# Kernel tuning notes

Hardware: AMD Instinct MI355X
Metric: run time of the kernel (lower is better)

Reference implementation:

```python
import jax, jax.numpy as jnp
import numpy as np

D_MODEL = 512
N_HEADS = 8
D_HEAD = 64
D_FF = 1024
EPS = 1e-5


def setup_inputs() -> dict:
    key = jax.random.key(0)
    ks = jax.random.split(key, 9)
    B, L = 4, 2048
    s = lambda fan_in: 1.0 / np.sqrt(fan_in)
    return {
        "x": jax.random.normal(ks[0], (B, L, D_MODEL), dtype=jnp.float32),
        "ln1_w": jnp.ones((D_MODEL,), jnp.float32),
        "ln1_b": jnp.zeros((D_MODEL,), jnp.float32),
        "ln2_w": jnp.ones((D_MODEL,), jnp.float32),
        "ln2_b": jnp.zeros((D_MODEL,), jnp.float32),
        "wq": jax.random.normal(ks[1], (D_MODEL, N_HEADS * D_HEAD), jnp.float32) * s(D_MODEL),
        "wk": jax.random.normal(ks[2], (D_MODEL, N_HEADS * D_HEAD), jnp.float32) * s(D_MODEL),
        "wv": jax.random.normal(ks[3], (D_MODEL, N_HEADS * D_HEAD), jnp.float32) * s(D_MODEL),
        "wo": jax.random.normal(ks[4], (N_HEADS * D_HEAD, D_MODEL), jnp.float32) * s(N_HEADS * D_HEAD),
        "w_gate": jax.random.normal(ks[5], (D_MODEL, D_FF), jnp.float32) * s(D_MODEL),
        "w_up": jax.random.normal(ks[6], (D_MODEL, D_FF), jnp.float32) * s(D_MODEL),
        "w_down": jax.random.normal(ks[7], (D_FF, D_MODEL), jnp.float32) * s(D_FF),
    }


def _layernorm(x, w, b):
    mu = jnp.mean(x, axis=-1, keepdims=True)
    var = jnp.var(x, axis=-1, keepdims=True)
    return (x - mu) * jax.lax.rsqrt(var + EPS) * w + b


def reference(x, ln1_w, ln1_b, ln2_w, ln2_b, wq, wk, wv, wo, w_gate, w_up, w_down):
    B, L, _ = x.shape
    scale = D_HEAD ** -0.5

    # --- attention sublayer (pre-LN residual) ---
    h = _layernorm(x, ln1_w, ln1_b)
    q = (h @ wq).reshape(B, L, N_HEADS, D_HEAD)  # [B,L,H,Dh]
    k = (h @ wk).reshape(B, L, N_HEADS, D_HEAD)
    v = (h @ wv).reshape(B, L, N_HEADS, D_HEAD)
    scores = jnp.einsum("bqhd,bkhd->bhqk", q, k) * scale
    # softmax computed in fp32, cast back (matches F.softmax(dtype=float32).to(q.dtype))
    attn = jax.nn.softmax(scores.astype(jnp.float32), axis=-1).astype(q.dtype)
    out = jnp.einsum("bhqk,bkhd->bqhd", attn, v).reshape(B, L, N_HEADS * D_HEAD)
    x = x + out @ wo

    # --- SwiGLU FFN sublayer (pre-LN residual) ---
    h = _layernorm(x, ln2_w, ln2_b)
    gate = jax.nn.silu(h @ w_gate)
    x = x + (gate * (h @ w_up)) @ w_down
    return x
```

## Files before the change

### kernel.cpp

```cpp
#include <hip/hip_runtime.h>
#include <hip/hip_bf16.h>
#include <math.h>

#define EPS 1e-5f

typedef __attribute__((ext_vector_type(8))) short bf16x8;
typedef __attribute__((ext_vector_type(4))) float f32x4;

__device__ __forceinline__ short f2bf(float x) {
    union { float f; unsigned u; } un; un.f = x;
    unsigned r = un.u + 0x7FFF + ((un.u >> 16) & 1);
    return (short)(r >> 16);
}
__device__ __forceinline__ float bf2f(short s) {
    union { unsigned u; float f; } un;
    un.u = ((unsigned)(unsigned short)s) << 16;
    return un.f;
}
__device__ __forceinline__ unsigned pack_bf2(float a, float b) {
    unsigned r;
    asm("v_cvt_pk_bf16_f32 %0, %1, %2" : "=v"(r) : "v"(a), "v"(b));
    return r;
}
__device__ __forceinline__ float exp2_fast(float x) {
    float r;
    asm("v_exp_f32 %0, %1" : "=v"(r) : "v"(x));
    return r;
}
__device__ __forceinline__ void load_lds16(const short* g, short* l) {
    __builtin_amdgcn_global_load_lds(
        (const __attribute__((address_space(1))) unsigned int*)g,
        (__attribute__((address_space(3))) unsigned int*)l, 16, 0, 0);
}

__global__ __launch_bounds__(256) void ln_kernel_b(const float* __restrict__ in,
                                                   const float* __restrict__ w,
                                                   const float* __restrict__ bb,
                                                   short* __restrict__ out) {
    int wv = threadIdx.x >> 6, lane = threadIdx.x & 63;
    int row = blockIdx.x * 4 + wv;
    const float* x = in + (size_t)row * 512 + lane * 8;
    float4 v0 = *(const float4*)x;
    float4 v1 = *(const float4*)(x + 4);
    float s  = (v0.x + v0.y) + (v0.z + v0.w) + (v1.x + v1.y) + (v1.z + v1.w);
    float s2 = v0.x*v0.x + v0.y*v0.y + v0.z*v0.z + v0.w*v0.w
             + v1.x*v1.x + v1.y*v1.y + v1.z*v1.z + v1.w*v1.w;
#pragma unroll
    for (int off = 1; off < 64; off <<= 1) {
        s  += __shfl_xor(s, off);
        s2 += __shfl_xor(s2, off);
    }
    float mu = s * (1.f / 512.f);
    float rstd = rsqrtf(s2 * (1.f / 512.f) - mu * mu + EPS);
    const float4 wa = *(const float4*)&w[lane * 8];
    const float4 wb = *(const float4*)&w[lane * 8 + 4];
    const float4 ba = *(const float4*)&bb[lane * 8];
    const float4 bv = *(const float4*)&bb[lane * 8 + 4];
    uint4 o;
    o.x = pack_bf2((v0.x - mu) * rstd * wa.x + ba.x, (v0.y - mu) * rstd * wa.y + ba.y);
    o.y = pack_bf2((v0.z - mu) * rstd * wa.z + ba.z, (v0.w - mu) * rstd * wa.w + ba.w);
    o.z = pack_bf2((v1.x - mu) * rstd * wb.x + bv.x, (v1.y - mu) * rstd * wb.y + bv.y);
    o.w = pack_bf2((v1.z - mu) * rstd * wb.z + bv.z, (v1.w - mu) * rstd * wb.w + bv.w);
    *(uint4*)&out[(size_t)row * 512 + lane * 8] = o;
}

struct WT { const float* w; short* t; int K; int N; };
struct WT7 { WT a[7]; };
__global__ __launch_bounds__(256) void transp_w_kernel(WT7 p) {
    WT e = p.a[blockIdx.z];
    int k0 = blockIdx.x * 32, n0 = blockIdx.y * 32;
    if (k0 >= e.K || n0 >= e.N) return;
    __shared__ short t[32][33];
    int tx = threadIdx.x & 31, ty = threadIdx.x >> 5;
#pragma unroll
    for (int pp = 0; pp < 4; pp++)
        t[pp * 8 + ty][tx] = f2bf(e.w[(size_t)(k0 + pp * 8 + ty) * e.N + n0 + tx]);
    __syncthreads();
#pragma unroll
    for (int pp = 0; pp < 4; pp++)
        e.t[(size_t)(n0 + pp * 8 + ty) * e.K + k0 + tx] = t[tx][pp * 8 + ty];
}

template <int EPI>
__global__ __launch_bounds__(256) void gemm_mfma(const short* __restrict__ A,
                                                 const short* __restrict__ Bt,
                                                 const float* __restrict__ res,
                                                 const short* __restrict__ resb,
                                                 void* __restrict__ Cv,
                                                 int M, int N, int K) {
    __shared__ short As[128 * 64];
    __shared__ short Bs[128 * 64];
    const int tid = threadIdx.x;
    const int lane = tid & 63, w = tid >> 6;
    const int g = lane >> 4, r16 = lane & 15;
    const int wr = w >> 1, wc = w & 1;

    const int nb = gridDim.x * gridDim.y;
    const int fid = blockIdx.y * gridDim.x + blockIdx.x;
    const int nid = (fid & 7) * (nb >> 3) + (fid >> 3);
    const int m0 = (nid / gridDim.x) * 128, n0 = (nid % gridDim.x) * 128;

    const int lr = lane >> 3;
    const int ck = (lane & 7) ^ lr;
    const int row0 = w * 32;

    f32x4 acc[4][4] = {};

    for (int k0 = 0; k0 < K; k0 += 64) {
        __syncthreads();
#pragma unroll
        for (int p = 0; p < 4; p++) {
            int rb = row0 + p * 8;
            load_lds16(&A [(size_t)(m0 + rb + lr) * K + k0 + ck * 8], &As[rb * 64]);
            load_lds16(&Bt[(size_t)(n0 + rb + lr) * K + k0 + ck * 8], &Bs[rb * 64]);
        }
        __syncthreads();
#pragma unroll
        for (int ks = 0; ks < 2; ks++) {
            bf16x8 av[4], bv[4];
#pragma unroll
            for (int i = 0; i < 4; i++) {
                int row = wr * 64 + i * 16 + r16;
                av[i] = *(const bf16x8*)&As[row * 64 + ((ks * 4 + g) ^ (row & 7)) * 8];
            }
#pragma unroll
            for (int j = 0; j < 4; j++) {
                int row = wc * 64 + j * 16 + r16;
                bv[j] = *(const bf16x8*)&Bs[row * 64 + ((ks * 4 + g) ^ (row & 7)) * 8];
            }
#pragma unroll
            for (int i = 0; i < 4; i++)
#pragma unroll
                for (int j = 0; j < 4; j++)
                    acc[i][j] = __builtin_amdgcn_mfma_f32_16x16x32_bf16(av[i], bv[j], acc[i][j], 0, 0, 0);
        }
    }

#pragma unroll
    for (int i = 0; i < 4; i++)
#pragma unroll
        for (int j = 0; j < 4; j++)
#pragma unroll
            for (int jr = 0; jr < 4; jr++) {
                int m = m0 + wr * 64 + i * 16 + 4 * g + jr;
                int n = n0 + wc * 64 + j * 16 + r16;
                float v = acc[i][j][jr];
                if (EPI == 0) {
                    size_t idx = (size_t)m * N + n;
                    ((float*)Cv)[idx] = res[idx] + v;
                } else if (EPI == 1) {
                    ((short*)Cv)[(size_t)m * N + n] = f2bf(v);
                } else if (EPI == 2) {
                    if (n < 512) v *= 0.18033688011112042f;
                    ((short*)Cv)[(size_t)(n >> 9) * 4194304 +
                                 (((size_t)(m >> 11) * 8 + ((n >> 6) & 7)) * 2048 + (m & 2047)) * 64 + (n & 63)] = f2bf(v);
                } else {
                    float gt = bf2f(resb[(size_t)m * N + n]);
                    float y = gt / (1.f + __expf(-gt)) * v;
                    ((short*)Cv)[(size_t)m * N + n] = f2bf(y);
                }
            }
}

__global__ __launch_bounds__(256) void transp_v_kernel(const short* __restrict__ vb,
                                                       short* __restrict__ vt) {
    __shared__ short tile[64][65];
    int l0 = blockIdx.x * 64;
    int bh = blockIdx.y;
    const size_t base = (size_t)bh * 2048 * 64;
    int tid = threadIdx.x;
#pragma unroll
    for (int p = 0; p < 4; p++) {
        int r = p * 16 + (tid >> 4);
        int c4 = (tid & 15) * 4;
        *(short4*)&tile[r][c4] = *(const short4*)&vb[base + (size_t)(l0 + r) * 64 + c4];
    }
    __syncthreads();
#pragma unroll
    for (int p = 0; p < 4; p++) {
        int d = p * 16 + (tid >> 4);
        int c4 = (tid & 15) * 4;
        short4 o;
        o.x = tile[c4 + 0][d]; o.y = tile[c4 + 1][d];
        o.z = tile[c4 + 2][d]; o.w = tile[c4 + 3][d];
        *(short4*)&vt[base + (size_t)d * 2048 + l0 + c4] = o;
    }
}

__global__ __launch_bounds__(256) void attn_mfma_kernel(const short* __restrict__ qb,
                                                        const short* __restrict__ kb,
                                                        const short* __restrict__ vt,
                                                        short* __restrict__ outb) {
    __shared__ short QP[128 * 64];
    __shared__ short Ks[2][4096];
    __shared__ short Vs[2][4096];

    const int fid = blockIdx.y * gridDim.x + blockIdx.x;
    const int nid = (fid & 7) * 64 + (fid >> 3);
    const int bh = nid >> 4, qt = nid & 15;
    const int b = bh >> 3, h = bh & 7;
    const int q0 = qt * 128;
    const size_t hb = (size_t)bh * (2048 * 64);

    const int tid = threadIdx.x;
    const int lane = tid & 63, w = tid >> 6;
    const int g = lane >> 4, r16 = lane & 15;
    const int lr = lane >> 3, ck = (lane & 7) ^ lr;
    const int rx = r16 & 7;

#pragma unroll
    for (int p = 0; p < 4; p++)
        load_lds16(&qb[hb + (size_t)(q0 + 32 * w + 8 * p + lr) * 64 + ck * 8],
                   &QP[(32 * w + 8 * p) * 64]);

    auto stageKV = [&](int buf, int kt) {
        int k0 = kt * 64;
        int rb = w * 16;
        load_lds16(&kb[hb + (size_t)(k0 + rb + lr) * 64 + ck * 8],      &Ks[buf][rb * 64]);
        load_lds16(&kb[hb + (size_t)(k0 + rb + 8 + lr) * 64 + ck * 8],  &Ks[buf][(rb + 8) * 64]);
        load_lds16(&vt[hb + (size_t)(rb + lr) * 2048 + k0 + ck * 8],     &Vs[buf][rb * 64]);
        load_lds16(&vt[hb + (size_t)(rb + 8 + lr) * 2048 + k0 + ck * 8], &Vs[buf][(rb + 8) * 64]);
    };
    stageKV(0, 0);

    bf16x8 aqA0, aqA1, aqB0, aqB1;
    float mA = -1e30f, lA = 0.f, mB = -1e30f, lB = 0.f;
    f32x4 oA[4] = {}, oB[4] = {};
    int cur = 0;

    for (int t = 0; t < 32; t++) {
        __syncthreads();
        if (t == 0) {
            int rowA = 32 * w + r16, rowB = rowA + 16;
            aqA0 = *(const bf16x8*)&QP[rowA * 64 + ((0 + g) ^ rx) * 8];
            aqA1 = *(const bf16x8*)&QP[rowA * 64 + ((4 + g) ^ rx) * 8];
            aqB0 = *(const bf16x8*)&QP[rowB * 64 + ((0 + g) ^ rx) * 8];
            aqB1 = *(const bf16x8*)&QP[rowB * 64 + ((4 + g) ^ rx) * 8];
        }
        if (t + 1 < 32) stageKV(cur ^ 1, t + 1);
        const short* Kc = &Ks[cur][0];
        const short* Vc = &Vs[cur][0];

        f32x4 sA[4], sB[4];
#pragma unroll
        for (int c = 0; c < 4; c++) {
            int row = 16 * c + r16;
            bf16x8 ak0 = *(const bf16x8*)&Kc[row * 64 + ((0 + g) ^ rx) * 8];
            bf16x8 ak1 = *(const bf16x8*)&Kc[row * 64 + ((4 + g) ^ rx) * 8];
            f32x4 a1 = {}, a2 = {};
            a1 = __builtin_amdgcn_mfma_f32_16x16x32_bf16(ak0, aqA0, a1, 0, 0, 0);
            a1 = __builtin_amdgcn_mfma_f32_16x16x32_bf16(ak1, aqA1, a1, 0, 0, 0);
            a2 = __builtin_amdgcn_mfma_f32_16x16x32_bf16(ak0, aqB0, a2, 0, 0, 0);
            a2 = __builtin_amdgcn_mfma_f32_16x16x32_bf16(ak1, aqB1, a2, 0, 0, 0);
            sA[c] = a1; sB[c] = a2;
        }

        float pmA = sA[0][0], pmB = sB[0][0];
#pragma unroll
        for (int c = 0; c < 4; c++)
#pragma unroll
            for (int jr = 0; jr < 4; jr++) {
                if (c || jr) {
                    pmA = fmaxf(pmA, sA[c][jr]);
                    pmB = fmaxf(pmB, sB[c][jr]);
                }
            }
        pmA = fmaxf(pmA, __shfl_xor(pmA, 16));
        pmA = fmaxf(pmA, __shfl_xor(pmA, 32));
        pmB = fmaxf(pmB, __shfl_xor(pmB, 16));
        pmB = fmaxf(pmB, __shfl_xor(pmB, 32));
        if (!__all((pmA - mA <= 8.f) && (pmB - mB <= 8.f))) {
            float mnA = fmaxf(mA, pmA), mnB = fmaxf(mB, pmB);
            float alA = exp2_fast(mA - mnA), alB = exp2_fast(mB - mnB);
            lA *= alA; lB *= alB;
#pragma unroll
            for (int c = 0; c < 4; c++) { oA[c] *= alA; oB[c] *= alB; }
            mA = mnA; mB = mnB;
        }
        float rsA = 0.f, rsB = 0.f;
        int prA = 32 * w + r16, prB = prA + 16;
#pragma unroll
        for (int c = 0; c < 4; c++) {
            int colbase = 16 * c + 4 * g;
            int co = (((colbase >> 3) ^ rx) * 8) + (colbase & 7);
            {
                float p0 = exp2_fast(sA[c][0] - mA), p1 = exp2_fast(sA[c][1] - mA);
                float p2 = exp2_fast(sA[c][2] - mA), p3 = exp2_fast(sA[c][3] - mA);
                rsA += (p0 + p1) + (p2 + p3);
                unsigned long long pv = (unsigned long long)pack_bf2(p0, p1)
                                      | ((unsigned long long)pack_bf2(p2, p3) << 32);
                *(unsigned long long*)&QP[prA * 64 + co] = pv;
            }
            {
                float p0 = exp2_fast(sB[c][0] - mB), p1 = exp2_fast(sB[c][1] - mB);
                float p2 = exp2_fast(sB[c][2] - mB), p3 = exp2_fast(sB[c][3] - mB);
                rsB += (p0 + p1) + (p2 + p3);
                unsigned long long pv = (unsigned long long)pack_bf2(p0, p1)
                                      | ((unsigned long long)pack_bf2(p2, p3) << 32);
                *(unsigned long long*)&QP[prB * 64 + co] = pv;
            }
        }
        rsA += __shfl_xor(rsA, 16); rsA += __shfl_xor(rsA, 32); lA += rsA;
        rsB += __shfl_xor(rsB, 16); rsB += __shfl_xor(rsB, 32); lB += rsB;

        bf16x8 bpA0 = *(const bf16x8*)&QP[prA * 64 + ((0 + g) ^ rx) * 8];
        bf16x8 bpA1 = *(const bf16x8*)&QP[prA * 64 + ((4 + g) ^ rx) * 8];
        bf16x8 bpB0 = *(const bf16x8*)&QP[prB * 64 + ((0 + g) ^ rx) * 8];
        bf16x8 bpB1 = *(const bf16x8*)&QP[prB * 64 + ((4 + g) ^ rx) * 8];
#pragma unroll
        for (int c = 0; c < 4; c++) {
            int row = 16 * c + r16;
            bf16x8 av0 = *(const bf16x8*)&Vc[row * 64 + ((0 + g) ^ rx) * 8];
            bf16x8 av1 = *(const bf16x8*)&Vc[row * 64 + ((4 + g) ^ rx) * 8];
            oA[c] = __builtin_amdgcn_mfma_f32_16x16x32_bf16(av0, bpA0, oA[c], 0, 0, 0);
            oA[c] = __builtin_amdgcn_mfma_f32_16x16x32_bf16(av1, bpA1, oA[c], 0, 0, 0);
            oB[c] = __builtin_amdgcn_mfma_f32_16x16x32_bf16(av0, bpB0, oB[c], 0, 0, 0);
            oB[c] = __builtin_amdgcn_mfma_f32_16x16x32_bf16(av1, bpB1, oB[c], 0, 0, 0);
        }
        cur ^= 1;
    }

    float ivA = 1.f / lA, ivB = 1.f / lB;
    int qa = q0 + 32 * w + r16;
#pragma unroll
    for (int c = 0; c < 4; c++) {
        int d = 16 * c + 4 * g;
        {
            unsigned long long pv = (unsigned long long)pack_bf2(oA[c][0] * ivA, oA[c][1] * ivA)
                                  | ((unsigned long long)pack_bf2(oA[c][2] * ivA, oA[c][3] * ivA) << 32);
            *(unsigned long long*)&outb[((size_t)b * 2048 + qa) * 512 + h * 64 + d] = pv;
        }
        {
            unsigned long long pv = (unsigned long long)pack_bf2(oB[c][0] * ivB, oB[c][1] * ivB)
                                  | ((unsigned long long)pack_bf2(oB[c][2] * ivB, oB[c][3] * ivB) << 32);
            *(unsigned long long*)&outb[((size_t)b * 2048 + qa + 16) * 512 + h * 64 + d] = pv;
        }
    }
}

extern "C" void kernel_launch(void* const* d_in, const int* in_sizes, int n_in,
                              void* d_out, int out_size, void* d_ws, size_t ws_size,
                              hipStream_t stream) {
    const float* x      = (const float*)d_in[0];
    const float* ln1_w  = (const float*)d_in[1];
    const float* ln1_b  = (const float*)d_in[2];
    const float* ln2_w  = (const float*)d_in[3];
    const float* ln2_b  = (const float*)d_in[4];
    const float* wq     = (const float*)d_in[5];
    const float* wk     = (const float*)d_in[6];
    const float* wv     = (const float*)d_in[7];
    const float* wo     = (const float*)d_in[8];
    const float* w_gate = (const float*)d_in[9];
    const float* w_up   = (const float*)d_in[10];
    const float* w_down = (const float*)d_in[11];
    float* out = (float*)d_out;

    const int M = 4 * 2048;
    char* ws = (char*)d_ws;
    const size_t MB = 1 << 20;
    short* h1b   = (short*)(ws);
    short* qb    = (short*)(ws + 8 * MB);
    short* kb    = (short*)(ws + 16 * MB);
    short* vb    = (short*)(ws + 24 * MB);
    short* vt    = (short*)(ws + 32 * MB);
    short* aob   = (short*)(ws + 40 * MB);
    short* g_b   = (short*)(ws + 48 * MB);
    short* u_b   = (short*)(ws + 64 * MB);
    short* qkvT  = (short*)(ws + 80 * MB);
    short* woT   = (short*)(ws + 82 * MB);
    short* wguT  = (short*)(ws + 83 * MB);
    short* wdT   = (short*)(ws + 85 * MB);
    short* h2b   = qb;

    WT7 wt;
    wt.a[0] = {wq,     qkvT,               512,  512};
    wt.a[1] = {wk,     qkvT + 512 * 512,   512,  512};
    wt.a[2] = {wv,     qkvT + 1024 * 512,  512,  512};
    wt.a[3] = {wo,     woT,                512,  512};
    wt.a[4] = {w_gate, wguT,               512, 1024};
    wt.a[5] = {w_up,   wguT + 1024 * 512,  512, 1024};
    wt.a[6] = {w_down, wdT,               1024,  512};

    transp_w_kernel<<<dim3(32, 32, 7), 256, 0, stream>>>(wt);
    ln_kernel_b<<<M / 4, 256, 0, stream>>>(x, ln1_w, ln1_b, h1b);
    gemm_mfma<2><<<dim3(12, 64), 256, 0, stream>>>(h1b, qkvT, nullptr, nullptr, qb, M, 1536, 512);
    transp_v_kernel<<<dim3(32, 32), 256, 0, stream>>>(vb, vt);
    attn_mfma_kernel<<<dim3(16, 32), 256, 0, stream>>>(qb, kb, vt, aob);
    gemm_mfma<0><<<dim3(4, 64), 256, 0, stream>>>(aob, woT, x, nullptr, out, M, 512, 512);
    ln_kernel_b<<<M / 4, 256, 0, stream>>>(out, ln2_w, ln2_b, h2b);
    gemm_mfma<1><<<dim3(8, 64), 256, 0, stream>>>(h2b, wguT, nullptr, nullptr, g_b, M, 1024, 512);
    gemm_mfma<4><<<dim3(8, 64), 256, 0, stream>>>(h2b, wguT + 1024 * 512, nullptr, g_b, u_b, M, 1024, 512);
    gemm_mfma<0><<<dim3(4, 64), 256, 0, stream>>>(u_b, wdT, out, nullptr, out, M, 512, 1024);
}
```

Before: 183.1 us.

## Double-buffer GEMM LDS tiles and software-pipeline attention PV MFMAs

The GEMM kernel now double-buffers its A/B LDS tiles and prefetches the next K tile while computing the current one, with one waitcnt+barrier per iteration instead of two syncthreads. The attention kernel defers the P·V MFMAs to the next iteration, holding V fragments and P in registers so they overlap with the next QK^T and softmax. It also drops the lazy-rescale threshold and always rescales. The cost is higher register and LDS pressure, which may lower occupancy, plus an unconditional rescale every tile.

```diff
diff --git a/kernel.cpp b/kernel.cpp
--- a/kernel.cpp
+++ b/kernel.cpp
@@ -6,6 +6,8 @@
 
 typedef __attribute__((ext_vector_type(8))) short bf16x8;
 typedef __attribute__((ext_vector_type(4))) float f32x4;
+
+#define MFMA16 __builtin_amdgcn_mfma_f32_16x16x32_bf16
 
 __device__ __forceinline__ short f2bf(float x) {
     union { float f; unsigned u; } un; un.f = x;
@@ -31,6 +33,11 @@
     __builtin_amdgcn_global_load_lds(
         (const __attribute__((address_space(1))) unsigned int*)g,
         (__attribute__((address_space(3))) unsigned int*)l, 16, 0, 0);
+}
+__device__ __forceinline__ void wait_vm0_barrier() {
+    asm volatile("s_waitcnt vmcnt(0)" ::: "memory");
+    __builtin_amdgcn_s_barrier();
+    __builtin_amdgcn_sched_barrier(0);
 }
 
 __global__ __launch_bounds__(256) void ln_kernel_b(const float* __restrict__ in,
@@ -88,8 +95,8 @@
                                                  const short* __restrict__ resb,
                                                  void* __restrict__ Cv,
                                                  int M, int N, int K) {
-    __shared__ short As[128 * 64];
-    __shared__ short Bs[128 * 64];
+    __shared__ short As[2][128 * 64];
+    __shared__ short Bs[2][128 * 64];
     const int tid = threadIdx.x;
     const int lane = tid & 63, w = tid >> 6;
     const int g = lane >> 4, r16 = lane & 15;
@@ -104,36 +111,44 @@
     const int ck = (lane & 7) ^ lr;
     const int row0 = w * 32;
 
-    f32x4 acc[4][4] = {};
-
-    for (int k0 = 0; k0 < K; k0 += 64) {
-        __syncthreads();
+    auto stage = [&](int buf, int k0) {
 #pragma unroll
         for (int p = 0; p < 4; p++) {
             int rb = row0 + p * 8;
-            load_lds16(&A [(size_t)(m0 + rb + lr) * K + k0 + ck * 8], &As[rb * 64]);
-            load_lds16(&Bt[(size_t)(n0 + rb + lr) * K + k0 + ck * 8], &Bs[rb * 64]);
-        }
-        __syncthreads();
+            load_lds16(&A [(size_t)(m0 + rb + lr) * K + k0 + ck * 8], &As[buf][rb * 64]);
+            load_lds16(&Bt[(size_t)(n0 + rb + lr) * K + k0 + ck * 8], &Bs[buf][rb * 64]);
+        }
+    };
+
+    f32x4 acc[4][4] = {};
+    stage(0, 0);
+    wait_vm0_barrier();
+
+    const int nt = K >> 6;
+    int cur = 0;
+    for (int t = 0; t < nt; t++) {
+        if (t + 1 < nt) stage(cur ^ 1, (t + 1) << 6);
 #pragma unroll
         for (int ks = 0; ks < 2; ks++) {
             bf16x8 av[4], bv[4];
 #pragma unroll
             for (int i = 0; i < 4; i++) {
                 int row = wr * 64 + i * 16 + r16;
-                av[i] = *(const bf16x8*)&As[row * 64 + ((ks * 4 + g) ^ (row & 7)) * 8];
+                av[i] = *(const bf16x8*)&As[cur][row * 64 + ((ks * 4 + g) ^ (row & 7)) * 8];
             }
 #pragma unroll
             for (int j = 0; j < 4; j++) {
                 int row = wc * 64 + j * 16 + r16;
-                bv[j] = *(const bf16x8*)&Bs[row * 64 + ((ks * 4 + g) ^ (row & 7)) * 8];
+                bv[j] = *(const bf16x8*)&Bs[cur][row * 64 + ((ks * 4 + g) ^ (row & 7)) * 8];
             }
 #pragma unroll
             for (int i = 0; i < 4; i++)
 #pragma unroll
                 for (int j = 0; j < 4; j++)
-                    acc[i][j] = __builtin_amdgcn_mfma_f32_16x16x32_bf16(av[i], bv[j], acc[i][j], 0, 0, 0);
-        }
+                    acc[i][j] = MFMA16(av[i], bv[j], acc[i][j], 0, 0, 0);
+        }
+        wait_vm0_barrier();
+        cur ^= 1;
     }
 
 #pragma unroll
@@ -222,21 +237,22 @@
         load_lds16(&vt[hb + (size_t)(rb + 8 + lr) * 2048 + k0 + ck * 8], &Vs[buf][(rb + 8) * 64]);
     };
     stageKV(0, 0);
-
-    bf16x8 aqA0, aqA1, aqB0, aqB1;
+    wait_vm0_barrier();
+
+    const int rowA = 32 * w + r16, rowB = rowA + 16;
+    bf16x8 aqA0 = *(const bf16x8*)&QP[rowA * 64 + ((0 + g) ^ rx) * 8];
+    bf16x8 aqA1 = *(const bf16x8*)&QP[rowA * 64 + ((4 + g) ^ rx) * 8];
+    bf16x8 aqB0 = *(const bf16x8*)&QP[rowB * 64 + ((0 + g) ^ rx) * 8];
+    bf16x8 aqB1 = *(const bf16x8*)&QP[rowB * 64 + ((4 + g) ^ rx) * 8];
+
     float mA = -1e30f, lA = 0.f, mB = -1e30f, lB = 0.f;
+    float alA = 1.f, alB = 1.f;
     f32x4 oA[4] = {}, oB[4] = {};
+    bf16x8 vf0, vf1, vf2, vf3, vf4, vf5, vf6, vf7;
+    bf16x8 pfA0, pfA1, pfB0, pfB1;
     int cur = 0;
 
     for (int t = 0; t < 32; t++) {
-        __syncthreads();
-        if (t == 0) {
-            int rowA = 32 * w + r16, rowB = rowA + 16;
-            aqA0 = *(const bf16x8*)&QP[rowA * 64 + ((0 + g) ^ rx) * 8];
-            aqA1 = *(const bf16x8*)&QP[rowA * 64 + ((4 + g) ^ rx) * 8];
-            aqB0 = *(const bf16x8*)&QP[rowB * 64 + ((0 + g) ^ rx) * 8];
-            aqB1 = *(const bf16x8*)&QP[rowB * 64 + ((4 + g) ^ rx) * 8];
-        }
         if (t + 1 < 32) stageKV(cur ^ 1, t + 1);
         const short* Kc = &Ks[cur][0];
         const short* Vc = &Vs[cur][0];
@@ -248,37 +264,49 @@
             bf16x8 ak0 = *(const bf16x8*)&Kc[row * 64 + ((0 + g) ^ rx) * 8];
             bf16x8 ak1 = *(const bf16x8*)&Kc[row * 64 + ((4 + g) ^ rx) * 8];
             f32x4 a1 = {}, a2 = {};
-            a1 = __builtin_amdgcn_mfma_f32_16x16x32_bf16(ak0, aqA0, a1, 0, 0, 0);
-            a1 = __builtin_amdgcn_mfma_f32_16x16x32_bf16(ak1, aqA1, a1, 0, 0, 0);
-            a2 = __builtin_amdgcn_mfma_f32_16x16x32_bf16(ak0, aqB0, a2, 0, 0, 0);
-            a2 = __builtin_amdgcn_mfma_f32_16x16x32_bf16(ak1, aqB1, a2, 0, 0, 0);
+            a1 = MFMA16(ak0, aqA0, a1, 0, 0, 0);
+            a1 = MFMA16(ak1, aqA1, a1, 0, 0, 0);
+            a2 = MFMA16(ak0, aqB0, a2, 0, 0, 0);
+            a2 = MFMA16(ak1, aqB1, a2, 0, 0, 0);
             sA[c] = a1; sB[c] = a2;
         }
 
-        float pmA = sA[0][0], pmB = sB[0][0];
-#pragma unroll
-        for (int c = 0; c < 4; c++)
-#pragma unroll
-            for (int jr = 0; jr < 4; jr++) {
-                if (c || jr) {
-                    pmA = fmaxf(pmA, sA[c][jr]);
-                    pmB = fmaxf(pmB, sB[c][jr]);
-                }
-            }
-        pmA = fmaxf(pmA, __shfl_xor(pmA, 16));
-        pmA = fmaxf(pmA, __shfl_xor(pmA, 32));
-        pmB = fmaxf(pmB, __shfl_xor(pmB, 16));
-        pmB = fmaxf(pmB, __shfl_xor(pmB, 32));
-        if (!__all((pmA - mA <= 8.f) && (pmB - mB <= 8.f))) {
-            float mnA = fmaxf(mA, pmA), mnB = fmaxf(mB, pmB);
-            float alA = exp2_fast(mA - mnA), alB = exp2_fast(mB - mnB);
-            lA *= alA; lB *= alB;
+        if (t > 0) {
 #pragma unroll
             for (int c = 0; c < 4; c++) { oA[c] *= alA; oB[c] *= alB; }
-            mA = mnA; mB = mnB;
-        }
+            oA[0] = MFMA16(vf0, pfA0, oA[0], 0, 0, 0); oA[0] = MFMA16(vf1, pfA1, oA[0], 0, 0, 0);
+            oB[0] = MFMA16(vf0, pfB0, oB[0], 0, 0, 0); oB[0] = MFMA16(vf1, pfB1, oB[0], 0, 0, 0);
+            oA[1] = MFMA16(vf2, pfA0, oA[1], 0, 0, 0); oA[1] = MFMA16(vf3, pfA1, oA[1], 0, 0, 0);
+            oB[1] = MFMA16(vf2, pfB0, oB[1], 0, 0, 0); oB[1] = MFMA16(vf3, pfB1, oB[1], 0, 0, 0);
+            oA[2] = MFMA16(vf4, pfA0, oA[2], 0, 0, 0); oA[2] = MFMA16(vf5, pfA1, oA[2], 0, 0, 0);
+            oB[2] = MFMA16(vf4, pfB0, oB[2], 0, 0, 0); oB[2] = MFMA16(vf5, pfB1, oB[2], 0, 0, 0);
+            oA[3] = MFMA16(vf6, pfA0, oA[3], 0, 0, 0); oA[3] = MFMA16(vf7, pfA1, oA[3], 0, 0, 0);
+            oB[3] = MFMA16(vf6, pfB0, oB[3], 0, 0, 0); oB[3] = MFMA16(vf7, pfB1, oB[3], 0, 0, 0);
+        }
+
+        vf0 = *(const bf16x8*)&Vc[(r16     ) * 64 + ((0 + g) ^ rx) * 8];
+        vf1 = *(const bf16x8*)&Vc[(r16     ) * 64 + ((4 + g) ^ rx) * 8];
+        vf2 = *(const bf16x8*)&Vc[(16 + r16) * 64 + ((0 + g) ^ rx) * 8];
+        vf3 = *(const bf16x8*)&Vc[(16 + r16) * 64 + ((4 + g) ^ rx) * 8];
+        vf4 = *(const bf16x8*)&Vc[(32 + r16) * 64 + ((0 + g) ^ rx) * 8];
+        vf5 = *(const bf16x8*)&Vc[(32 + r16) * 64 + ((4 + g) ^ rx) * 8];
+        vf6 = *(const bf16x8*)&Vc[(48 + r16) * 64 + ((0 + g) ^ rx) * 8];
+        vf7 = *(const bf16x8*)&Vc[(48 + r16) * 64 + ((4 + g) ^ rx) * 8];
+
+        float pmA = fmaxf(fmaxf(sA[0][0], sA[0][1]), fmaxf(sA[0][2], sA[0][3]));
+        float pmB = fmaxf(fmaxf(sB[0][0], sB[0][1]), fmaxf(sB[0][2], sB[0][3]));
+#pragma unroll
+        for (int c = 1; c < 4; c++) {
+            pmA = fmaxf(pmA, fmaxf(fmaxf(sA[c][0], sA[c][1]), fmaxf(sA[c][2], sA[c][3])));
+            pmB = fmaxf(pmB, fmaxf(fmaxf(sB[c][0], sB[c][1]), fmaxf(sB[c][2], sB[c][3])));
+        }
+        pmA = fmaxf(pmA, __shfl_xor(pmA, 16)); pmA = fmaxf(pmA, __shfl_xor(pmA, 32));
+        pmB = fmaxf(pmB, __shfl_xor(pmB, 16)); pmB = fmaxf(pmB, __shfl_xor(pmB, 32));
+        float mnA = fmaxf(mA, pmA), mnB = fmaxf(mB, pmB);
+        alA = exp2_fast(mA - mnA); alB = exp2_fast(mB - mnB);
+        mA = mnA; mB = mnB;
+        lA *= alA; lB *= alB;
         float rsA = 0.f, rsB = 0.f;
-        int prA = 32 * w + r16, prB = prA + 16;
 #pragma unroll
         for (int c = 0; c < 4; c++) {
             int colbase = 16 * c + 4 * g;
@@ -289,7 +317,7 @@
                 rsA += (p0 + p1) + (p2 + p3);
                 unsigned long long pv = (unsigned long long)pack_bf2(p0, p1)
                                       | ((unsigned long long)pack_bf2(p2, p3) << 32);
-                *(unsigned long long*)&QP[prA * 64 + co] = pv;
+                *(unsigned long long*)&QP[rowA * 64 + co] = pv;
             }
             {
                 float p0 = exp2_fast(sB[c][0] - mB), p1 = exp2_fast(sB[c][1] - mB);
@@ -297,28 +325,31 @@
                 rsB += (p0 + p1) + (p2 + p3);
                 unsigned long long pv = (unsigned long long)pack_bf2(p0, p1)
                                       | ((unsigned long long)pack_bf2(p2, p3) << 32);
-                *(unsigned long long*)&QP[prB * 64 + co] = pv;
+                *(unsigned long long*)&QP[rowB * 64 + co] = pv;
             }
         }
         rsA += __shfl_xor(rsA, 16); rsA += __shfl_xor(rsA, 32); lA += rsA;
         rsB += __shfl_xor(rsB, 16); rsB += __shfl_xor(rsB, 32); lB += rsB;
 
-        bf16x8 bpA0 = *(const bf16x8*)&QP[prA * 64 + ((0 + g) ^ rx) * 8];
-        bf16x8 bpA1 = *(const bf16x8*)&QP[prA * 64 + ((4 + g) ^ rx) * 8];
-        bf16x8 bpB0 = *(const bf16x8*)&QP[prB * 64 + ((0 + g) ^ rx) * 8];
-        bf16x8 bpB1 = *(const bf16x8*)&QP[prB * 64 + ((4 + g) ^ rx) * 8];
-#pragma unroll
-        for (int c = 0; c < 4; c++) {
-            int row = 16 * c + r16;
-            bf16x8 av0 = *(const bf16x8*)&Vc[row * 64 + ((0 + g) ^ rx) * 8];
-            bf16x8 av1 = *(const bf16x8*)&Vc[row * 64 + ((4 + g) ^ rx) * 8];
-            oA[c] = __builtin_amdgcn_mfma_f32_16x16x32_bf16(av0, bpA0, oA[c], 0, 0, 0);
-            oA[c] = __builtin_amdgcn_mfma_f32_16x16x32_bf16(av1, bpA1, oA[c], 0, 0, 0);
-            oB[c] = __builtin_amdgcn_mfma_f32_16x16x32_bf16(av0, bpB0, oB[c], 0, 0, 0);
-            oB[c] = __builtin_amdgcn_mfma_f32_16x16x32_bf16(av1, bpB1, oB[c], 0, 0, 0);
-        }
+        pfA0 = *(const bf16x8*)&QP[rowA * 64 + ((0 + g) ^ rx) * 8];
+        pfA1 = *(const bf16x8*)&QP[rowA * 64 + ((4 + g) ^ rx) * 8];
+        pfB0 = *(const bf16x8*)&QP[rowB * 64 + ((0 + g) ^ rx) * 8];
+        pfB1 = *(const bf16x8*)&QP[rowB * 64 + ((4 + g) ^ rx) * 8];
+
+        wait_vm0_barrier();
         cur ^= 1;
     }
+
+#pragma unroll
+    for (int c = 0; c < 4; c++) { oA[c] *= alA; oB[c] *= alB; }
+    oA[0] = MFMA16(vf0, pfA0, oA[0], 0, 0, 0); oA[0] = MFMA16(vf1, pfA1, oA[0], 0, 0, 0);
+    oB[0] = MFMA16(vf0, pfB0, oB[0], 0, 0, 0); oB[0] = MFMA16(vf1, pfB1, oB[0], 0, 0, 0);
+    oA[1] = MFMA16(vf2, pfA0, oA[1], 0, 0, 0); oA[1] = MFMA16(vf3, pfA1, oA[1], 0, 0, 0);
+    oB[1] = MFMA16(vf2, pfB0, oB[1], 0, 0, 0); oB[1] = MFMA16(vf3, pfB1, oB[1], 0, 0, 0);
+    oA[2] = MFMA16(vf4, pfA0, oA[2], 0, 0, 0); oA[2] = MFMA16(vf5, pfA1, oA[2], 0, 0, 0);
+    oB[2] = MFMA16(vf4, pfB0, oB[2], 0, 0, 0); oB[2] = MFMA16(vf5, pfB1, oB[2], 0, 0, 0);
+    oA[3] = MFMA16(vf6, pfA0, oA[3], 0, 0, 0); oA[3] = MFMA16(vf7, pfA1, oA[3], 0, 0, 0);
+    oB[3] = MFMA16(vf6, pfB0, oB[3], 0, 0, 0); oB[3] = MFMA16(vf7, pfB1, oB[3], 0, 0, 0);
 
     float ivA = 1.f / lA, ivB = 1.f / lB;
     int qa = q0 + 32 * w + r16;
```

After: 188.1 us. +2.7%, slower.
